# Optimization experiments

Measured on AMD Instinct MI355X. Metric: run time of the kernel, lower is better.

The kernel has to match this reference:

```python
import jax, jax.numpy as jnp
import numpy as np

N_NODES = 250000
N_EDGES = 5000000


def setup_inputs() -> dict:
    key = jax.random.key(0)
    k1, k2, k3, k4, k5, k6 = jax.random.split(key, 6)
    x = jax.random.normal(k1, (N_NODES, 1), dtype=jnp.float32)
    edge_index = jax.random.randint(k2, (2, N_EDGES), 0, N_NODES, dtype=jnp.int64)
    # Glorot-style small weights like PyG GCNConv init
    W1 = jax.random.normal(k3, (1, 16), dtype=jnp.float32) * (1.0 / np.sqrt(1 + 16))
    b1 = jnp.zeros((16,), dtype=jnp.float32)
    W2 = jax.random.normal(k4, (16, 2), dtype=jnp.float32) * (1.0 / np.sqrt(16 + 2))
    b2 = jnp.zeros((2,), dtype=jnp.float32)
    return {"x": x, "edge_index": edge_index, "W1": W1, "b1": b1, "W2": W2, "b2": b2}


def _gcn_conv(x, row, col, W, b, n_nodes):
    """PyG GCNConv: x' = D^{-1/2} (A + I) D^{-1/2} (x W) + b.

    row = source nodes, col = target nodes (messages flow row -> col).
    Self-loops are assumed already appended to row/col.
    """
    h = x @ W  # [N, out]
    ones = jnp.ones(row.shape[0], dtype=h.dtype)
    deg = jax.ops.segment_sum(ones, col, num_segments=n_nodes)  # in-degree incl. self-loop
    dinv = jnp.where(deg > 0, jax.lax.rsqrt(deg), 0.0)
    norm = dinv[row] * dinv[col]  # [E+N]
    msg = h[row] * norm[:, None]  # gather + scale  [E+N, out]
    out = jax.ops.segment_sum(msg, col, num_segments=n_nodes)  # scatter-add
    return out + b


def reference(x, edge_index, W1, b1, W2, b2):
    n = x.shape[0]
    loop = jnp.arange(n, dtype=edge_index.dtype)
    row = jnp.concatenate([edge_index[0], loop])
    col = jnp.concatenate([edge_index[1], loop])
    h = _gcn_conv(x, row, col, W1, b1, n)
    h = jax.nn.relu(h)
    # F.dropout(training=False) at inference -> identity
    h = _gcn_conv(h, row, col, W2, b2, n)
    return jax.nn.softmax(h, axis=1)
```

## Files before the change

### kernel.cpp

```cpp
#include <hip/hip_runtime.h>

#define ST 1024
#define PT 20
#define EPB (ST * PT)
#define CSHIFT 10
#define CMASK 1023u
#define CW 1024
#define CAP 24576


__global__ void k_init(unsigned* __restrict__ gcur, int NC) {
    for (int b = threadIdx.x; b < NC; b += blockDim.x)
        gcur[b] = (unsigned)b * CAP;
}

__global__ __launch_bounds__(ST) void k_sort(const int* __restrict__ row,
                                             const int* __restrict__ col,
                                             unsigned* __restrict__ gcur,
                                             unsigned* __restrict__ pack1,
                                             int E, int NC) {
    __shared__ unsigned cnt[CW];
    __shared__ unsigned cur[CW];
    int t = threadIdx.x;
    cnt[t] = 0;
    __syncthreads();

    int base = blockIdx.x * EPB;
    int c[PT];

#pragma unroll
    for (int k = 0; k < PT / 4; ++k) {
        int e = base + (k * ST + t) * 4;
        int4 cc;
        if (e + 3 < E) {
            cc = *reinterpret_cast<const int4*>(col + e);
        } else {
            cc.x = (e + 0 < E) ? col[e + 0] : -1;
            cc.y = (e + 1 < E) ? col[e + 1] : -1;
            cc.z = (e + 2 < E) ? col[e + 2] : -1;
            cc.w = (e + 3 < E) ? col[e + 3] : -1;
        }
        c[4 * k + 0] = cc.x; c[4 * k + 1] = cc.y;
        c[4 * k + 2] = cc.z; c[4 * k + 3] = cc.w;
    }
#pragma unroll
    for (int k = 0; k < PT; ++k)
        if (c[k] >= 0) atomicAdd(&cnt[(unsigned)c[k] >> CSHIFT], 1u);
    __syncthreads();

    if (t < NC) cur[t] = atomicAdd(&gcur[t], cnt[t]);
    __syncthreads();

#pragma unroll
    for (int k = 0; k < PT / 4; ++k) {
        int e = base + (k * ST + t) * 4;
        int4 rr;
        if (e + 3 < E) {
            rr = *reinterpret_cast<const int4*>(row + e);
        } else {
            rr.x = (e + 0 < E) ? row[e + 0] : 0;
            rr.y = (e + 1 < E) ? row[e + 1] : 0;
            rr.z = (e + 2 < E) ? row[e + 2] : 0;
            rr.w = (e + 3 < E) ? row[e + 3] : 0;
        }
        int rl[4] = {rr.x, rr.y, rr.z, rr.w};
#pragma unroll
        for (int j = 0; j < 4; ++j) {
            int cc = c[4 * k + j];
            if (cc >= 0) {
                unsigned b = (unsigned)cc >> CSHIFT;
                unsigned pos = atomicAdd(&cur[b], 1u);
                if (pos < (b + 1u) * CAP)
                    pack1[pos] = ((unsigned)rl[j] << CSHIFT) | ((unsigned)cc & CMASK);
            }
        }
    }
}

__global__ void k_deg(const unsigned* __restrict__ pack1, const unsigned* __restrict__ gcur,
                      const float* __restrict__ x,
                      float* __restrict__ dinv, float* __restrict__ xs, int N) {
    __shared__ unsigned dcnt[CW];
    int b = blockIdx.x;
    int t = threadIdx.x;
    dcnt[t] = 0;
    __syncthreads();
    unsigned s0 = (unsigned)b * CAP;
    unsigned s1 = min(gcur[b], s0 + CAP);
    unsigned n4 = (s1 - s0) >> 2;
    for (unsigned i = t; i < n4; i += CW) {
        uint4 p = reinterpret_cast<const uint4*>(pack1 + s0)[i];
        atomicAdd(&dcnt[p.x & CMASK], 1u);
        atomicAdd(&dcnt[p.y & CMASK], 1u);
        atomicAdd(&dcnt[p.z & CMASK], 1u);
        atomicAdd(&dcnt[p.w & CMASK], 1u);
    }
    unsigned i = s0 + (n4 << 2) + t;
    if (i < s1) atomicAdd(&dcnt[pack1[i] & CMASK], 1u);
    __syncthreads();
    int v = (b << CSHIFT) + t;
    if (v < N) {
        float di = rsqrtf((float)dcnt[t] + 1.0f);
        dinv[v] = di;
        xs[v] = di * x[v];
    }
}

__global__ void k_l1(const unsigned* __restrict__ pack1, const unsigned* __restrict__ gcur,
                     const float* __restrict__ xs, const float* __restrict__ dinv,
                     const float* __restrict__ W1, const float* __restrict__ b1,
                     const float* __restrict__ W2,
                     float* __restrict__ gs, int N) {
    __shared__ float acc[CW];
    int b = blockIdx.x;
    int t = threadIdx.x;
    acc[t] = 0.0f;
    __syncthreads();
    unsigned s0 = (unsigned)b * CAP;
    unsigned s1 = min(gcur[b], s0 + CAP);
    unsigned n4 = (s1 - s0) >> 2;
    for (unsigned i = t; i < n4; i += CW) {
        uint4 p = reinterpret_cast<const uint4*>(pack1 + s0)[i];
        float v0 = xs[p.x >> CSHIFT];
        float v1 = xs[p.y >> CSHIFT];
        float v2 = xs[p.z >> CSHIFT];
        float v3 = xs[p.w >> CSHIFT];
        atomicAdd(&acc[p.x & CMASK], v0);
        atomicAdd(&acc[p.y & CMASK], v1);
        atomicAdd(&acc[p.z & CMASK], v2);
        atomicAdd(&acc[p.w & CMASK], v3);
    }
    unsigned i = s0 + (n4 << 2) + t;
    if (i < s1) {
        unsigned p = pack1[i];
        atomicAdd(&acc[p & CMASK], xs[p >> CSHIFT]);
    }
    __syncthreads();
    int v = (b << CSHIFT) + t;
    if (v < N) {
        float di = dinv[v];
        float tt = di * (acc[t] + xs[v]);
        float g = 0.0f;
#pragma unroll
        for (int j = 0; j < 16; ++j) {
            float y = fmaxf(fmaf(W1[j], tt, b1[j]), 0.0f);
            g = fmaf(W2[2 * j] - W2[2 * j + 1], y, g);
        }
        gs[v] = di * g;
    }
}

__global__ void k_l2(const unsigned* __restrict__ pack1, const unsigned* __restrict__ gcur,
                     const float* __restrict__ gs, const float* __restrict__ dinv,
                     const float* __restrict__ b2,
                     float* __restrict__ out, int N) {
    __shared__ float acc[CW];
    int b = blockIdx.x;
    int t = threadIdx.x;
    acc[t] = 0.0f;
    __syncthreads();
    unsigned s0 = (unsigned)b * CAP;
    unsigned s1 = min(gcur[b], s0 + CAP);
    unsigned n4 = (s1 - s0) >> 2;
    for (unsigned i = t; i < n4; i += CW) {
        uint4 p = reinterpret_cast<const uint4*>(pack1 + s0)[i];
        float v0 = gs[p.x >> CSHIFT];
        float v1 = gs[p.y >> CSHIFT];
        float v2 = gs[p.z >> CSHIFT];
        float v3 = gs[p.w >> CSHIFT];
        atomicAdd(&acc[p.x & CMASK], v0);
        atomicAdd(&acc[p.y & CMASK], v1);
        atomicAdd(&acc[p.z & CMASK], v2);
        atomicAdd(&acc[p.w & CMASK], v3);
    }
    unsigned i = s0 + (n4 << 2) + t;
    if (i < s1) {
        unsigned p = pack1[i];
        atomicAdd(&acc[p & CMASK], gs[p >> CSHIFT]);
    }
    __syncthreads();
    int v = (b << CSHIFT) + t;
    if (v < N) {
        float diff = dinv[v] * (acc[t] + gs[v]) + (b2[0] - b2[1]);
        float p0 = 1.0f / (1.0f + __expf(-diff));
        float2 o;
        o.x = p0;
        o.y = 1.0f - p0;
        reinterpret_cast<float2*>(out)[v] = o;
    }
}

__global__ void k_zero_f(float* __restrict__ p, int n) {
    int i = blockIdx.x * blockDim.x + threadIdx.x;
    int v = i * 4;
    if (v + 3 < n) {
        reinterpret_cast<float4*>(p + v)[0] = make_float4(0.f, 0.f, 0.f, 0.f);
    } else {
        for (; v < n; ++v) p[v] = 0.0f;
    }
}
__global__ void k_deg_f(const int* __restrict__ col, float* __restrict__ deg, int E) {
    int i = blockIdx.x * blockDim.x + threadIdx.x;
    int e = i * 4;
    if (e + 3 < E) {
        int4 c = reinterpret_cast<const int4*>(col + e)[0];
        atomicAdd(deg + c.x, 1.0f); atomicAdd(deg + c.y, 1.0f);
        atomicAdd(deg + c.z, 1.0f); atomicAdd(deg + c.w, 1.0f);
    } else {
        for (; e < E; ++e) atomicAdd(deg + col[e], 1.0f);
    }
}
__global__ void k_node1_f(const float* __restrict__ x, float* __restrict__ degdinv,
                          float* __restrict__ xs, int N) {
    int v = blockIdx.x * blockDim.x + threadIdx.x;
    if (v < N) {
        float dinv = rsqrtf(degdinv[v] + 1.0f);
        degdinv[v] = dinv;
        xs[v] = dinv * x[v];
    }
}
__global__ void k_scat_f(const int* __restrict__ row, const int* __restrict__ col,
                         const float* __restrict__ src, float* __restrict__ acc, int E) {
    int i = blockIdx.x * blockDim.x + threadIdx.x;
    int e = i * 4;
    if (e + 3 < E) {
        int4 r = reinterpret_cast<const int4*>(row + e)[0];
        int4 c = reinterpret_cast<const int4*>(col + e)[0];
        float s0 = src[r.x], s1 = src[r.y], s2 = src[r.z], s3 = src[r.w];
        atomicAdd(acc + c.x, s0); atomicAdd(acc + c.y, s1);
        atomicAdd(acc + c.z, s2); atomicAdd(acc + c.w, s3);
    } else {
        for (; e < E; ++e) atomicAdd(acc + col[e], src[row[e]]);
    }
}
__global__ void k_mlp_f(const float* __restrict__ W1, const float* __restrict__ b1,
                        const float* __restrict__ W2, const float* __restrict__ dinv,
                        float* __restrict__ acc, float* __restrict__ xsgs, int N) {
    int v = blockIdx.x * blockDim.x + threadIdx.x;
    if (v < N) {
        float di = dinv[v];
        float t = di * (acc[v] + xsgs[v]);
        float g = 0.0f;
#pragma unroll
        for (int j = 0; j < 16; ++j) {
            float y = fmaxf(fmaf(W1[j], t, b1[j]), 0.0f);
            g = fmaf(W2[2 * j] - W2[2 * j + 1], y, g);
        }
        xsgs[v] = di * g;
        acc[v] = 0.0f;
    }
}
__global__ void k_out_f(const float* __restrict__ b2, const float* __restrict__ dinv,
                        const float* __restrict__ acc, const float* __restrict__ gs,
                        float* __restrict__ out, int N) {
    int v = blockIdx.x * blockDim.x + threadIdx.x;
    if (v < N) {
        float diff = dinv[v] * (acc[v] + gs[v]) + (b2[0] - b2[1]);
        float p0 = 1.0f / (1.0f + __expf(-diff));
        float2 o; o.x = p0; o.y = 1.0f - p0;
        reinterpret_cast<float2*>(out)[v] = o;
    }
}

extern "C" void kernel_launch(void* const* d_in, const int* in_sizes, int n_in,
                              void* d_out, int out_size, void* d_ws, size_t ws_size,
                              hipStream_t stream) {
    const float* x  = (const float*)d_in[0];
    const int* edge = (const int*)d_in[1];
    const float* W1 = (const float*)d_in[2];
    const float* b1 = (const float*)d_in[3];
    const float* W2 = (const float*)d_in[4];
    const float* b2 = (const float*)d_in[5];
    float* out = (float*)d_out;

    const int N = in_sizes[0];
    const int E = in_sizes[1] / 2;
    const int* row = edge;
    const int* col = edge + E;

    const int NC  = (N + CW - 1) >> CSHIFT;
    const int NBS = (E + EPB - 1) / EPB;

    const double mean = (double)E / NC;
    const double slack = mean + 8.0 * __builtin_sqrt(mean);
    const size_t need = ((size_t)NC * CAP + NC) * 4 + (size_t)3 * N * 4;

    const int nb = (N + 255) / 256;

    if (NC <= 1024 && N < (1 << 22) && slack < CAP && ws_size >= need) {
        unsigned* pack1 = (unsigned*)d_ws;
        unsigned* gcur  = pack1 + (size_t)NC * CAP;
        float* dinv     = (float*)(gcur + NC);
        float* xs       = dinv + N;
        float* gs       = xs + N;

        k_init<<<1, 256, 0, stream>>>(gcur, NC);
        k_sort<<<NBS, ST, 0, stream>>>(row, col, gcur, pack1, E, NC);
        k_deg <<<NC, CW, 0, stream>>>(pack1, gcur, x, dinv, xs, N);
        k_l1  <<<NC, CW, 0, stream>>>(pack1, gcur, xs, dinv, W1, b1, W2, gs, N);
        k_l2  <<<NC, CW, 0, stream>>>(pack1, gcur, gs, dinv, b2, out, N);
    } else {
        float* w0 = (float*)d_ws;
        float* w1 = w0 + N;
        float* w2 = w1 + N;
        const int eb = ((E + 3) / 4 + 255) / 256;
        const int zb = ((2 * N + 3) / 4 + 255) / 256;
        k_zero_f <<<zb, 256, 0, stream>>>(w0, 2 * N);
        k_deg_f  <<<eb, 256, 0, stream>>>(col, w0, E);
        k_node1_f<<<nb, 256, 0, stream>>>(x, w0, w2, N);
        k_scat_f <<<eb, 256, 0, stream>>>(row, col, w2, w1, E);
        k_mlp_f  <<<nb, 256, 0, stream>>>(W1, b1, W2, w0, w1, w2, N);
        k_scat_f <<<eb, 256, 0, stream>>>(row, col, w2, w1, E);
        k_out_f  <<<nb, 256, 0, stream>>>(b2, w0, w1, w2, out, N);
    }
}
```

Before: 181.2 us.

## Fuse sort, degree and both GCN layers into one cooperative kernel

Result: slower. 684.0 us (+277.5%).

```diff
diff --git a/kernel.cpp b/kernel.cpp
--- a/kernel.cpp
+++ b/kernel.cpp
@@ -1,33 +1,28 @@
 #include <hip/hip_runtime.h>
-
-#define ST 1024
+#include <hip/hip_cooperative_groups.h>
+
+namespace cg = cooperative_groups;
+
+#define ST 512
 #define PT 20
 #define EPB (ST * PT)
-#define CSHIFT 10
-#define CMASK 1023u
-#define CW 1024
-#define CAP 24576
-
-
-__global__ void k_init(unsigned* __restrict__ gcur, int NC) {
-    for (int b = threadIdx.x; b < NC; b += blockDim.x)
-        gcur[b] = (unsigned)b * CAP;
-}
-
-__global__ __launch_bounds__(ST) void k_sort(const int* __restrict__ row,
-                                             const int* __restrict__ col,
-                                             unsigned* __restrict__ gcur,
-                                             unsigned* __restrict__ pack1,
-                                             int E, int NC) {
+#define CSHIFT 9
+#define CMASK 511u
+#define CW 512
+#define CAP 12288
+
+
+__device__ __forceinline__ void sort_body(const int* __restrict__ row,
+                                          const int* __restrict__ col,
+                                          unsigned* __restrict__ gcur,
+                                          unsigned* __restrict__ pack1,
+                                          int E, int NC, int b, int t) {
     __shared__ unsigned cnt[CW];
     __shared__ unsigned cur[CW];
-    int t = threadIdx.x;
     cnt[t] = 0;
     __syncthreads();
-
-    int base = blockIdx.x * EPB;
+    int base = b * EPB;
     int c[PT];
-
 #pragma unroll
     for (int k = 0; k < PT / 4; ++k) {
         int e = base + (k * ST + t) * 4;
@@ -35,30 +30,27 @@
         if (e + 3 < E) {
             cc = *reinterpret_cast<const int4*>(col + e);
         } else {
-            cc.x = (e + 0 < E) ? col[e + 0] : -1;
+            cc.x = (e     < E) ? col[e]     : -1;
             cc.y = (e + 1 < E) ? col[e + 1] : -1;
             cc.z = (e + 2 < E) ? col[e + 2] : -1;
             cc.w = (e + 3 < E) ? col[e + 3] : -1;
         }
-        c[4 * k + 0] = cc.x; c[4 * k + 1] = cc.y;
-        c[4 * k + 2] = cc.z; c[4 * k + 3] = cc.w;
+        c[4 * k] = cc.x; c[4 * k + 1] = cc.y; c[4 * k + 2] = cc.z; c[4 * k + 3] = cc.w;
     }
 #pragma unroll
     for (int k = 0; k < PT; ++k)
         if (c[k] >= 0) atomicAdd(&cnt[(unsigned)c[k] >> CSHIFT], 1u);
     __syncthreads();
-
     if (t < NC) cur[t] = atomicAdd(&gcur[t], cnt[t]);
     __syncthreads();
-
 #pragma unroll
     for (int k = 0; k < PT / 4; ++k) {
         int e = base + (k * ST + t) * 4;
-        int4 rr;
+        int4 rr = make_int4(0, 0, 0, 0);
         if (e + 3 < E) {
             rr = *reinterpret_cast<const int4*>(row + e);
         } else {
-            rr.x = (e + 0 < E) ? row[e + 0] : 0;
+            rr.x = (e     < E) ? row[e]     : 0;
             rr.y = (e + 1 < E) ? row[e + 1] : 0;
             rr.z = (e + 2 < E) ? row[e + 2] : 0;
             rr.w = (e + 3 < E) ? row[e + 3] : 0;
@@ -68,27 +60,24 @@
         for (int j = 0; j < 4; ++j) {
             int cc = c[4 * k + j];
             if (cc >= 0) {
-                unsigned b = (unsigned)cc >> CSHIFT;
-                unsigned pos = atomicAdd(&cur[b], 1u);
-                if (pos < (b + 1u) * CAP)
+                unsigned bb = (unsigned)cc >> CSHIFT;
+                unsigned pos = atomicAdd(&cur[bb], 1u);
+                if (pos < (bb + 1u) * CAP)
                     pack1[pos] = ((unsigned)rl[j] << CSHIFT) | ((unsigned)cc & CMASK);
             }
         }
     }
 }
 
-__global__ void k_deg(const unsigned* __restrict__ pack1, const unsigned* __restrict__ gcur,
-                      const float* __restrict__ x,
-                      float* __restrict__ dinv, float* __restrict__ xs, int N) {
+__device__ __forceinline__ void deg_body(const unsigned* __restrict__ pack1,
+                                         const float* __restrict__ x,
+                                         float* __restrict__ dinv, float* __restrict__ xs,
+                                         unsigned s0, unsigned s1, int N, int b, int t) {
     __shared__ unsigned dcnt[CW];
-    int b = blockIdx.x;
-    int t = threadIdx.x;
     dcnt[t] = 0;
     __syncthreads();
-    unsigned s0 = (unsigned)b * CAP;
-    unsigned s1 = min(gcur[b], s0 + CAP);
     unsigned n4 = (s1 - s0) >> 2;
-    for (unsigned i = t; i < n4; i += CW) {
+    for (unsigned i = t; i < n4; i += ST) {
         uint4 p = reinterpret_cast<const uint4*>(pack1 + s0)[i];
         atomicAdd(&dcnt[p.x & CMASK], 1u);
         atomicAdd(&dcnt[p.y & CMASK], 1u);
@@ -106,20 +95,19 @@
     }
 }
 
-__global__ void k_l1(const unsigned* __restrict__ pack1, const unsigned* __restrict__ gcur,
-                     const float* __restrict__ xs, const float* __restrict__ dinv,
-                     const float* __restrict__ W1, const float* __restrict__ b1,
-                     const float* __restrict__ W2,
-                     float* __restrict__ gs, int N) {
+__device__ __forceinline__ void l1_body(const unsigned* __restrict__ pack1,
+                                        const float* __restrict__ xs,
+                                        const float* __restrict__ dinv,
+                                        const float* __restrict__ W1,
+                                        const float* __restrict__ b1,
+                                        const float* __restrict__ W2,
+                                        float* __restrict__ gs,
+                                        unsigned s0, unsigned s1, int N, int b, int t) {
     __shared__ float acc[CW];
-    int b = blockIdx.x;
-    int t = threadIdx.x;
     acc[t] = 0.0f;
     __syncthreads();
-    unsigned s0 = (unsigned)b * CAP;
-    unsigned s1 = min(gcur[b], s0 + CAP);
     unsigned n4 = (s1 - s0) >> 2;
-    for (unsigned i = t; i < n4; i += CW) {
+    for (unsigned i = t; i < n4; i += ST) {
         uint4 p = reinterpret_cast<const uint4*>(pack1 + s0)[i];
         float v0 = xs[p.x >> CSHIFT];
         float v1 = xs[p.y >> CSHIFT];
@@ -150,19 +138,17 @@
     }
 }
 
-__global__ void k_l2(const unsigned* __restrict__ pack1, const unsigned* __restrict__ gcur,
-                     const float* __restrict__ gs, const float* __restrict__ dinv,
-                     const float* __restrict__ b2,
-                     float* __restrict__ out, int N) {
+__device__ __forceinline__ void l2_body(const unsigned* __restrict__ pack1,
+                                        const float* __restrict__ gs,
+                                        const float* __restrict__ dinv,
+                                        const float* __restrict__ b2,
+                                        float* __restrict__ out,
+                                        unsigned s0, unsigned s1, int N, int b, int t) {
     __shared__ float acc[CW];
-    int b = blockIdx.x;
-    int t = threadIdx.x;
     acc[t] = 0.0f;
     __syncthreads();
-    unsigned s0 = (unsigned)b * CAP;
-    unsigned s1 = min(gcur[b], s0 + CAP);
     unsigned n4 = (s1 - s0) >> 2;
-    for (unsigned i = t; i < n4; i += CW) {
+    for (unsigned i = t; i < n4; i += ST) {
         uint4 p = reinterpret_cast<const uint4*>(pack1 + s0)[i];
         float v0 = gs[p.x >> CSHIFT];
         float v1 = gs[p.y >> CSHIFT];
@@ -188,6 +174,93 @@
         o.y = 1.0f - p0;
         reinterpret_cast<float2*>(out)[v] = o;
     }
+}
+
+__global__ __launch_bounds__(ST) void k_mega(const int* __restrict__ row,
+                                             const int* __restrict__ col,
+                                             const float* __restrict__ x,
+                                             const float* __restrict__ W1,
+                                             const float* __restrict__ b1,
+                                             const float* __restrict__ W2,
+                                             const float* __restrict__ b2,
+                                             unsigned* __restrict__ gcur,
+                                             unsigned* __restrict__ pack1,
+                                             float* __restrict__ dinv,
+                                             float* __restrict__ xs,
+                                             float* __restrict__ gs,
+                                             float* __restrict__ out,
+                                             int E, int N, int NC) {
+    cg::grid_group grid = cg::this_grid();
+    const int b = blockIdx.x;
+    const int t = threadIdx.x;
+
+    if (t == 0 && b < NC) gcur[b] = (unsigned)b * CAP;
+    grid.sync();
+
+    sort_body(row, col, gcur, pack1, E, NC, b, t);
+    __threadfence();
+    grid.sync();
+
+    unsigned s0 = 0, s1 = 0;
+    if (b < NC) {
+        s0 = (unsigned)b * CAP;
+        s1 = min(gcur[b], s0 + (unsigned)CAP);
+    }
+
+    if (b < NC) deg_body(pack1, x, dinv, xs, s0, s1, N, b, t);
+    __threadfence();
+    grid.sync();
+
+    if (b < NC) l1_body(pack1, xs, dinv, W1, b1, W2, gs, s0, s1, N, b, t);
+    __threadfence();
+    grid.sync();
+
+    if (b < NC) l2_body(pack1, gs, dinv, b2, out, s0, s1, N, b, t);
+}
+
+__global__ void k_init(unsigned* __restrict__ gcur, int NC) {
+    for (int b = threadIdx.x + blockIdx.x * blockDim.x; b < NC; b += blockDim.x * gridDim.x)
+        gcur[b] = (unsigned)b * CAP;
+}
+__global__ __launch_bounds__(ST) void k_sortk(const int* __restrict__ row,
+                                              const int* __restrict__ col,
+                                              unsigned* __restrict__ gcur,
+                                              unsigned* __restrict__ pack1, int E, int NC) {
+    sort_body(row, col, gcur, pack1, E, NC, blockIdx.x, threadIdx.x);
+}
+__global__ __launch_bounds__(ST) void k_degk(const unsigned* __restrict__ pack1,
+                                             const unsigned* __restrict__ gcur,
+                                             const float* __restrict__ x,
+                                             float* __restrict__ dinv, float* __restrict__ xs,
+                                             int N) {
+    int b = blockIdx.x;
+    unsigned s0 = (unsigned)b * CAP;
+    unsigned s1 = min(gcur[b], s0 + (unsigned)CAP);
+    deg_body(pack1, x, dinv, xs, s0, s1, N, b, threadIdx.x);
+}
+__global__ __launch_bounds__(ST) void k_l1k(const unsigned* __restrict__ pack1,
+                                            const unsigned* __restrict__ gcur,
+                                            const float* __restrict__ xs,
+                                            const float* __restrict__ dinv,
+                                            const float* __restrict__ W1,
+                                            const float* __restrict__ b1,
+                                            const float* __restrict__ W2,
+                                            float* __restrict__ gs, int N) {
+    int b = blockIdx.x;
+    unsigned s0 = (unsigned)b * CAP;
+    unsigned s1 = min(gcur[b], s0 + (unsigned)CAP);
+    l1_body(pack1, xs, dinv, W1, b1, W2, gs, s0, s1, N, b, threadIdx.x);
+}
+__global__ __launch_bounds__(ST) void k_l2k(const unsigned* __restrict__ pack1,
+                                            const unsigned* __restrict__ gcur,
+                                            const float* __restrict__ gs,
+                                            const float* __restrict__ dinv,
+                                            const float* __restrict__ b2,
+                                            float* __restrict__ out, int N) {
+    int b = blockIdx.x;
+    unsigned s0 = (unsigned)b * CAP;
+    unsigned s1 = min(gcur[b], s0 + (unsigned)CAP);
+    l2_body(pack1, gs, dinv, b2, out, s0, s1, N, b, threadIdx.x);
 }
 
 __global__ void k_zero_f(float* __restrict__ p, int n) {
@@ -280,29 +353,38 @@
 
     const int NC  = (N + CW - 1) >> CSHIFT;
     const int NBS = (E + EPB - 1) / EPB;
+    const int NB  = NC > NBS ? NC : NBS;
 
     const double mean = (double)E / NC;
-    const double slack = mean + 8.0 * __builtin_sqrt(mean);
+    const double slack = mean + 8.0 * __builtin_sqrt(mean > 1.0 ? mean : 1.0);
     const size_t need = ((size_t)NC * CAP + NC) * 4 + (size_t)3 * N * 4;
 
-    const int nb = (N + 255) / 256;
-
-    if (NC <= 1024 && N < (1 << 22) && slack < CAP && ws_size >= need) {
+    if (NC <= CW && N < (1 << 23) && slack < CAP && ws_size >= need) {
         unsigned* pack1 = (unsigned*)d_ws;
         unsigned* gcur  = pack1 + (size_t)NC * CAP;
         float* dinv     = (float*)(gcur + NC);
         float* xs       = dinv + N;
         float* gs       = xs + N;
 
-        k_init<<<1, 256, 0, stream>>>(gcur, NC);
-        k_sort<<<NBS, ST, 0, stream>>>(row, col, gcur, pack1, E, NC);
-        k_deg <<<NC, CW, 0, stream>>>(pack1, gcur, x, dinv, xs, N);
-        k_l1  <<<NC, CW, 0, stream>>>(pack1, gcur, xs, dinv, W1, b1, W2, gs, N);
-        k_l2  <<<NC, CW, 0, stream>>>(pack1, gcur, gs, dinv, b2, out, N);
+        void* args[] = {(void*)&row, (void*)&col, (void*)&x,
+                        (void*)&W1, (void*)&b1, (void*)&W2, (void*)&b2,
+                        (void*)&gcur, (void*)&pack1,
+                        (void*)&dinv, (void*)&xs, (void*)&gs, (void*)&out,
+                        (void*)&E, (void*)&N, (void*)&NC};
+        hipError_t err = hipLaunchCooperativeKernel((const void*)k_mega, dim3(NB), dim3(ST),
+                                                    args, 0, stream);
+        if (err != hipSuccess) {
+            k_init <<<1, 512, 0, stream>>>(gcur, NC);
+            k_sortk<<<NBS, ST, 0, stream>>>(row, col, gcur, pack1, E, NC);
+            k_degk <<<NC, ST, 0, stream>>>(pack1, gcur, x, dinv, xs, N);
+            k_l1k  <<<NC, ST, 0, stream>>>(pack1, gcur, xs, dinv, W1, b1, W2, gs, N);
+            k_l2k  <<<NC, ST, 0, stream>>>(pack1, gcur, gs, dinv, b2, out, N);
+        }
     } else {
         float* w0 = (float*)d_ws;
         float* w1 = w0 + N;
         float* w2 = w1 + N;
+        const int nb = (N + 255) / 256;
         const int eb = ((E + 3) / 4 + 255) / 256;
         const int zb = ((2 * N + 3) / 4 + 255) / 256;
         k_zero_f <<<zb, 256, 0, stream>>>(w0, 2 * N);
```
